# Optimization experiments

Measured on AMD Instinct MI355X. Metric: run time of the kernel, lower is better.

The kernel has to match this reference:

```python
import jax, jax.numpy as jnp
import numpy as np

B, C, L = 128, 1, 4096


def setup_inputs() -> dict:
    key = jax.random.key(0)
    x_0 = jax.random.normal(key, (B, C, L), dtype=jnp.float32)
    return {"x_0": x_0}


def reference(x_0):
    # Original: per-sample F.conv1d(x, flip(x), padding=L-1).
    # Cross-correlation with a flipped kernel == full linear convolution:
    #   out[b, t] = sum_c sum_i x[b,c,i] * x[b,c,t-i],  t in [0, 2L-2]
    # Vectorized over batch and channels via vmap; summed over channels
    # (conv1d contracts input channels against the weight's channel dim).
    conv = jax.vmap(jax.vmap(lambda a: jnp.convolve(a, a, mode='full')))(x_0)  # [B, C, 2L-1]
    return conv.sum(axis=1)[:, None, :]  # [B, 1, 2L-1]
```

## Files before the change

### kernel.cpp

```cpp
#include <hip/hip_runtime.h>

#define LL    4096
#define OUTL  8191
#define FPAD  272
#define NPDW  2336
#define CB1   2352
#define RB    4704
#define BTOP  5887
#define NGUP  992
#define LDSDW 9824
#define UNRL  17

typedef short v8s __attribute__((ext_vector_type(8)));
typedef float v4f __attribute__((ext_vector_type(4)));

__device__ __forceinline__ unsigned bf16b(float f) {
    unsigned u = __builtin_bit_cast(unsigned, f);
    u += 0x7fff + ((u >> 16) & 1);
    return u >> 16;
}
__device__ __forceinline__ unsigned pk(float lo, float hi) {
    return bf16b(lo) | (bf16b(hi) << 16);
}
__device__ __forceinline__ int swz(int g) { return g ^ (((g >> 3) & 3) << 1); }

__global__ __launch_bounds__(512, 4)
void selfconv_mfma7(const float* __restrict__ xg, float* __restrict__ outg) {
    __shared__ unsigned lds[LDSDW];
    const int tid = threadIdx.x;
    const int blk = blockIdx.x;
    const int b   = blk & 127;
    const int id  = blk >> 7;
    const int rg  = (id == 0) ? 0 : (id == 1) ? 3 : (id == 2) ? 1 : 2;
    const int T0  = rg << 11;
    const float* __restrict__ xb = xg + b * LL;

#pragma unroll
    for (int rr = 0; rr < 2; ++rr) {
        int w = tid + rr * 512;
        if (w < 584) {
            int E = 8 * w - FPAD;
            float e0,e1,e2,e3,e4,e5,e6,e7,e8;
            if (E >= 0 && E + 8 < LL) {
                float4 fa = *(const float4*)(xb + E);
                float4 fb = *(const float4*)(xb + E + 4);
                e0=fa.x; e1=fa.y; e2=fa.z; e3=fa.w;
                e4=fb.x; e5=fb.y; e6=fb.z; e7=fb.w; e8=xb[E+8];
            } else {
                float t[9];
#pragma unroll
                for (int k = 0; k < 9; ++k) {
                    int e = E + k;
                    t[k] = (e >= 0 && e < LL) ? xb[e] : 0.f;
                }
                e0=t[0]; e1=t[1]; e2=t[2]; e3=t[3]; e4=t[4];
                e5=t[5]; e6=t[6]; e7=t[7]; e8=t[8];
            }
            unsigned p0 = pk(e0, e1), p1 = pk(e2, e3);
            unsigned p2 = pk(e4, e5), p3 = pk(e6, e7);
            unsigned b8 = bf16b(e8);
            uint4 d0{p0, p1, p2, p3};
            uint4 d1{(p0 >> 16) | (p1 << 16), (p1 >> 16) | (p2 << 16),
                     (p2 >> 16) | (p3 << 16), (p3 >> 16) | (b8 << 16)};
            *(uint4*)&lds[4 * w]       = d0;
            *(uint4*)&lds[CB1 + 4 * w] = d1;
        }
    }
    {
        int g = 224 + tid;
        int x0 = BTOP - 7 - 8 * g;
        float4 fa = *(const float4*)(xb + x0);
        float4 fb = *(const float4*)(xb + x0 + 4);
        uint4 o{pk(fb.w, fb.z), pk(fb.y, fb.x), pk(fa.w, fa.z), pk(fa.y, fa.x)};
        *(uint4*)&lds[RB + 4 * swz(g)] = o;
    }
    if (tid < 480) {
        int u = (tid < 224) ? tid : tid + 512;
        *(uint4*)&lds[RB + 4 * u] = uint4{0, 0, 0, 0};
    }
    __syncthreads();

    const int wv = tid >> 6, lane = tid & 63, ln16 = lane & 15, q = lane >> 4;

    int mn = 0x7fffffff, mx = -0x7fffffff;
#pragma unroll
    for (int u = 0; u < 2; ++u)
#pragma unroll
        for (int v = 0; v < 4; ++v) {
            int base = T0 + 256 * u + 512 * v;
            int iLo = base - (LL - 1); if (iLo < 0) iLo = 0;
            int iHi = base + 255;      if (iHi > LL - 1) iHi = LL - 1;
            int a = iLo - 256 * u; if (a < mn) mn = a;
            int c2 = iHi - 256 * u; if (c2 > mx) mx = c2;
        }
    const int base_   = mn - 15;
    const int i0start = base_ - ((base_ - 1) & 7);
    const int nch     = ((mx - i0start) >> 5) + 1;
    const int nw      = (nch - wv + 7) >> 3;
    const int i0w     = i0start + 32 * wv;

    const int s0p = i0w + ln16 + 8 * q + FPAD;
    const int aw  = (s0p >> 1) + ((s0p & 1) ? CB1 : 0);
    const int g3 = (4352 - T0 + i0w - 16 * ln16 + 8 * q) >> 3;
    const int bw = RB + 4 * swz(g3);

    v4f a00{0,0,0,0}, a01{0,0,0,0}, a02{0,0,0,0}, a03{0,0,0,0};
    v4f a10{0,0,0,0}, a11{0,0,0,0}, a12{0,0,0,0}, a13{0,0,0,0};

    auto mkA = [](const unsigned* p) {
        union { unsigned x[4]; v8s s; } z;
        z.x[0] = p[0]; z.x[1] = p[1]; z.x[2] = p[2]; z.x[3] = p[3];
        return z.s;
    };
    auto mkB = [](uint4 v) {
        union { unsigned x[4]; v8s s; } z;
        z.x[0] = v.x; z.x[1] = v.y; z.x[2] = v.z; z.x[3] = v.w; return z.s;
    };

    uint4 Hb[8];
    unsigned Ab[3][4];
#pragma unroll
    for (int j = 0; j < 7; ++j) Hb[j] = *(const uint4*)&lds[bw + 128 * j];
    Hb[7] = uint4{0, 0, 0, 0};
#pragma unroll
    for (int k = 0; k < 4; ++k) {
        Ab[0][k] = lds[aw + k];
        Ab[1][k] = lds[aw + 128 + k];
        Ab[2][k] = 0u;
    }

#pragma unroll
    for (int t = 0; t < UNRL; ++t) {
        if (t < nw) {
            if (t + 1 < nw) {
                Hb[(t + 7) & 7] = *(const uint4*)&lds[bw + 128 * (t + 7)];
                const int an = aw + 128 * (t + 2);
#pragma unroll
                for (int k = 0; k < 4; ++k) Ab[(t + 2) % 3][k] = lds[an + k];
            }
            v8s A0 = mkA(Ab[t % 3]);
            v8s A1 = mkA(Ab[(t + 1) % 3]);
            v8s B3 = mkB(Hb[t & 7]),       B2 = mkB(Hb[(t + 2) & 7]);
            v8s B1 = mkB(Hb[(t + 4) & 7]), B0 = mkB(Hb[(t + 6) & 7]);
            __builtin_amdgcn_s_setprio(1);
            a03 = __builtin_amdgcn_mfma_f32_16x16x32_bf16(A0, B3, a03, 0, 0, 0);
            a13 = __builtin_amdgcn_mfma_f32_16x16x32_bf16(A1, B3, a13, 0, 0, 0);
            a02 = __builtin_amdgcn_mfma_f32_16x16x32_bf16(A0, B2, a02, 0, 0, 0);
            a12 = __builtin_amdgcn_mfma_f32_16x16x32_bf16(A1, B2, a12, 0, 0, 0);
            a01 = __builtin_amdgcn_mfma_f32_16x16x32_bf16(A0, B1, a01, 0, 0, 0);
            a11 = __builtin_amdgcn_mfma_f32_16x16x32_bf16(A1, B1, a11, 0, 0, 0);
            a00 = __builtin_amdgcn_mfma_f32_16x16x32_bf16(A0, B0, a00, 0, 0, 0);
            a10 = __builtin_amdgcn_mfma_f32_16x16x32_bf16(A1, B0, a10, 0, 0, 0);
            __builtin_amdgcn_s_setprio(0);
        }
    }

    float* fs = (float*)lds;
    __syncthreads();
    if (wv >= 4) {
        int sb = (wv - 4) * 2304 + lane * 36;
        *(v4f*)&fs[sb]      = a00; *(v4f*)&fs[sb + 4]  = a10;
        *(v4f*)&fs[sb + 8]  = a01; *(v4f*)&fs[sb + 12] = a11;
        *(v4f*)&fs[sb + 16] = a02; *(v4f*)&fs[sb + 20] = a12;
        *(v4f*)&fs[sb + 24] = a03; *(v4f*)&fs[sb + 28] = a13;
    }
    __syncthreads();
    if (wv < 4) {
        int sb = wv * 2304 + lane * 36;
        a00 += *(const v4f*)&fs[sb];      a10 += *(const v4f*)&fs[sb + 4];
        a01 += *(const v4f*)&fs[sb + 8];  a11 += *(const v4f*)&fs[sb + 12];
        a02 += *(const v4f*)&fs[sb + 16]; a12 += *(const v4f*)&fs[sb + 20];
        a03 += *(const v4f*)&fs[sb + 24]; a13 += *(const v4f*)&fs[sb + 28];
    }
    __syncthreads();
    if (wv >= 1 && wv < 4) {
        int sb = (wv - 1) * 2304 + lane * 36;
        *(v4f*)&fs[sb]      = a00; *(v4f*)&fs[sb + 4]  = a10;
        *(v4f*)&fs[sb + 8]  = a01; *(v4f*)&fs[sb + 12] = a11;
        *(v4f*)&fs[sb + 16] = a02; *(v4f*)&fs[sb + 20] = a12;
        *(v4f*)&fs[sb + 24] = a03; *(v4f*)&fs[sb + 28] = a13;
    }
    __syncthreads();
    if (wv == 0) {
#pragma unroll
        for (int s = 0; s < 3; ++s) {
            int sb = s * 2304 + lane * 36;
            a00 += *(const v4f*)&fs[sb];      a10 += *(const v4f*)&fs[sb + 4];
            a01 += *(const v4f*)&fs[sb + 8];  a11 += *(const v4f*)&fs[sb + 12];
            a02 += *(const v4f*)&fs[sb + 16]; a12 += *(const v4f*)&fs[sb + 20];
            a03 += *(const v4f*)&fs[sb + 24]; a13 += *(const v4f*)&fs[sb + 28];
        }
        float* __restrict__ ob = outg + b * OUTL;
        const v4f* accs[8] = {&a00, &a10, &a01, &a11, &a02, &a12, &a03, &a13};
#pragma unroll
        for (int uv = 0; uv < 8; ++uv) {
            int u = uv & 1, v = uv >> 1;
            int tilebase = T0 + 256 * u + 512 * v;
            int tb = tilebase + 4 * q + 16 * ln16;
            v4f a = *accs[uv];
            if (tilebase + 255 < OUTL) {
                *(v4f*)&ob[tb] = a;
            } else {
#pragma unroll
                for (int r2 = 0; r2 < 4; ++r2)
                    if (tb + r2 < OUTL) ob[tb + r2] = a[r2];
            }
        }
    }
}

extern "C" void kernel_launch(void* const* d_in, const int* in_sizes, int n_in,
                              void* d_out, int out_size, void* d_ws, size_t ws_size,
                              hipStream_t stream) {
    const float* x = (const float*)d_in[0];
    float* out = (float*)d_out;
    selfconv_mfma7<<<dim3(512), dim3(512), 0, stream>>>(x, out);
}
```

Measured before the change: 61.29 us.

## Replace serial tree reduction with all-wave parallel LDS reduction and store

The cross-wave accumulator reduction goes from a two-stage tree that ended with wave 0 doing all output stores to a single LDS dump by all eight waves. Each wave then sums one output tile across the eight partials and writes it to global memory. This removes two barriers and spreads the reduction and store work over every wave. It also rewrites the operand register buffers as v8s vectors. LDS grows to 64 KB per block, which may limit how many blocks fit per CU.

Measured after the change: 60.86 us. Within noise of the previous version (-0.7%).

```diff
diff --git a/kernel.cpp b/kernel.cpp
--- a/kernel.cpp
+++ b/kernel.cpp
@@ -7,8 +7,7 @@
 #define CB1   2352
 #define RB    4704
 #define BTOP  5887
-#define NGUP  992
-#define LDSDW 9824
+#define LDSDW 16384
 #define UNRL  17
 
 typedef short v8s __attribute__((ext_vector_type(8)));
@@ -25,7 +24,7 @@
 __device__ __forceinline__ int swz(int g) { return g ^ (((g >> 3) & 3) << 1); }
 
 __global__ __launch_bounds__(512, 4)
-void selfconv_mfma7(const float* __restrict__ xg, float* __restrict__ outg) {
+void selfconv_mfma8(const float* __restrict__ xg, float* __restrict__ outg) {
     __shared__ unsigned lds[LDSDW];
     const int tid = threadIdx.x;
     const int blk = blockIdx.x;
@@ -107,41 +106,31 @@
     v4f a00{0,0,0,0}, a01{0,0,0,0}, a02{0,0,0,0}, a03{0,0,0,0};
     v4f a10{0,0,0,0}, a11{0,0,0,0}, a12{0,0,0,0}, a13{0,0,0,0};
 
-    auto mkA = [](const unsigned* p) {
+    auto ldA = [&](int addr) -> v8s {
         union { unsigned x[4]; v8s s; } z;
-        z.x[0] = p[0]; z.x[1] = p[1]; z.x[2] = p[2]; z.x[3] = p[3];
+        z.x[0] = lds[addr];     z.x[1] = lds[addr + 1];
+        z.x[2] = lds[addr + 2]; z.x[3] = lds[addr + 3];
         return z.s;
     };
-    auto mkB = [](uint4 v) {
-        union { unsigned x[4]; v8s s; } z;
-        z.x[0] = v.x; z.x[1] = v.y; z.x[2] = v.z; z.x[3] = v.w; return z.s;
-    };
 
-    uint4 Hb[8];
-    unsigned Ab[3][4];
+    v8s Hs[8];
+    v8s Ah[3];
 #pragma unroll
-    for (int j = 0; j < 7; ++j) Hb[j] = *(const uint4*)&lds[bw + 128 * j];
-    Hb[7] = uint4{0, 0, 0, 0};
-#pragma unroll
-    for (int k = 0; k < 4; ++k) {
-        Ab[0][k] = lds[aw + k];
-        Ab[1][k] = lds[aw + 128 + k];
-        Ab[2][k] = 0u;
-    }
+    for (int j = 0; j < 7; ++j) Hs[j] = *(const v8s*)&lds[bw + 128 * j];
+    Ah[0] = ldA(aw);
+    Ah[1] = ldA(aw + 128);
 
 #pragma unroll
     for (int t = 0; t < UNRL; ++t) {
         if (t < nw) {
             if (t + 1 < nw) {
-                Hb[(t + 7) & 7] = *(const uint4*)&lds[bw + 128 * (t + 7)];
-                const int an = aw + 128 * (t + 2);
-#pragma unroll
-                for (int k = 0; k < 4; ++k) Ab[(t + 2) % 3][k] = lds[an + k];
+                Hs[(t + 7) & 7] = *(const v8s*)&lds[bw + 128 * (t + 7)];
+                Ah[(t + 2) % 3] = ldA(aw + 128 * (t + 2));
             }
-            v8s A0 = mkA(Ab[t % 3]);
-            v8s A1 = mkA(Ab[(t + 1) % 3]);
-            v8s B3 = mkB(Hb[t & 7]),       B2 = mkB(Hb[(t + 2) & 7]);
-            v8s B1 = mkB(Hb[(t + 4) & 7]), B0 = mkB(Hb[(t + 6) & 7]);
+            v8s A0 = Ah[t % 3];
+            v8s A1 = Ah[(t + 1) % 3];
+            v8s B3 = Hs[t & 7],       B2 = Hs[(t + 2) & 7];
+            v8s B1 = Hs[(t + 4) & 7], B0 = Hs[(t + 6) & 7];
             __builtin_amdgcn_s_setprio(1);
             a03 = __builtin_amdgcn_mfma_f32_16x16x32_bf16(A0, B3, a03, 0, 0, 0);
             a13 = __builtin_amdgcn_mfma_f32_16x16x32_bf16(A1, B3, a13, 0, 0, 0);
@@ -157,54 +146,31 @@
 
     float* fs = (float*)lds;
     __syncthreads();
-    if (wv >= 4) {
-        int sb = (wv - 4) * 2304 + lane * 36;
-        *(v4f*)&fs[sb]      = a00; *(v4f*)&fs[sb + 4]  = a10;
-        *(v4f*)&fs[sb + 8]  = a01; *(v4f*)&fs[sb + 12] = a11;
-        *(v4f*)&fs[sb + 16] = a02; *(v4f*)&fs[sb + 20] = a12;
-        *(v4f*)&fs[sb + 24] = a03; *(v4f*)&fs[sb + 28] = a13;
+    {
+        const int lb = wv * 256 + lane * 4;
+        *(v4f*)&fs[0 * 2048 + lb] = a00; *(v4f*)&fs[1 * 2048 + lb] = a10;
+        *(v4f*)&fs[2 * 2048 + lb] = a01; *(v4f*)&fs[3 * 2048 + lb] = a11;
+        *(v4f*)&fs[4 * 2048 + lb] = a02; *(v4f*)&fs[5 * 2048 + lb] = a12;
+        *(v4f*)&fs[6 * 2048 + lb] = a03; *(v4f*)&fs[7 * 2048 + lb] = a13;
     }
     __syncthreads();
-    if (wv < 4) {
-        int sb = wv * 2304 + lane * 36;
-        a00 += *(const v4f*)&fs[sb];      a10 += *(const v4f*)&fs[sb + 4];
-        a01 += *(const v4f*)&fs[sb + 8];  a11 += *(const v4f*)&fs[sb + 12];
-        a02 += *(const v4f*)&fs[sb + 16]; a12 += *(const v4f*)&fs[sb + 20];
-        a03 += *(const v4f*)&fs[sb + 24]; a13 += *(const v4f*)&fs[sb + 28];
-    }
-    __syncthreads();
-    if (wv >= 1 && wv < 4) {
-        int sb = (wv - 1) * 2304 + lane * 36;
-        *(v4f*)&fs[sb]      = a00; *(v4f*)&fs[sb + 4]  = a10;
-        *(v4f*)&fs[sb + 8]  = a01; *(v4f*)&fs[sb + 12] = a11;
-        *(v4f*)&fs[sb + 16] = a02; *(v4f*)&fs[sb + 20] = a12;
-        *(v4f*)&fs[sb + 24] = a03; *(v4f*)&fs[sb + 28] = a13;
-    }
-    __syncthreads();
-    if (wv == 0) {
+    {
+        v4f s{0, 0, 0, 0};
+        const int tb0 = wv * 2048 + lane * 4;
 #pragma unroll
-        for (int s = 0; s < 3; ++s) {
-            int sb = s * 2304 + lane * 36;
-            a00 += *(const v4f*)&fs[sb];      a10 += *(const v4f*)&fs[sb + 4];
-            a01 += *(const v4f*)&fs[sb + 8];  a11 += *(const v4f*)&fs[sb + 12];
-            a02 += *(const v4f*)&fs[sb + 16]; a12 += *(const v4f*)&fs[sb + 20];
-            a03 += *(const v4f*)&fs[sb + 24]; a13 += *(const v4f*)&fs[sb + 28];
-        }
+        for (int w = 0; w < 8; ++w)
+            s += *(const v4f*)&fs[tb0 + w * 256];
+
+        const int u = wv & 1, v = wv >> 1;
+        const int tilebase = T0 + 256 * u + 512 * v;
+        const int tb = tilebase + 16 * ln16 + 4 * q;
         float* __restrict__ ob = outg + b * OUTL;
-        const v4f* accs[8] = {&a00, &a10, &a01, &a11, &a02, &a12, &a03, &a13};
+        if (tilebase + 255 < OUTL) {
+            *(v4f*)&ob[tb] = s;
+        } else {
 #pragma unroll
-        for (int uv = 0; uv < 8; ++uv) {
-            int u = uv & 1, v = uv >> 1;
-            int tilebase = T0 + 256 * u + 512 * v;
-            int tb = tilebase + 4 * q + 16 * ln16;
-            v4f a = *accs[uv];
-            if (tilebase + 255 < OUTL) {
-                *(v4f*)&ob[tb] = a;
-            } else {
-#pragma unroll
-                for (int r2 = 0; r2 < 4; ++r2)
-                    if (tb + r2 < OUTL) ob[tb + r2] = a[r2];
-            }
+            for (int r2 = 0; r2 < 4; ++r2)
+                if (tb + r2 < OUTL) ob[tb + r2] = s[r2];
         }
     }
 }
@@ -214,5 +180,5 @@
                               hipStream_t stream) {
     const float* x = (const float*)d_in[0];
     float* out = (float*)d_out;
-    selfconv_mfma7<<<dim3(512), dim3(512), 0, stream>>>(x, out);
+    selfconv_mfma8<<<dim3(512), dim3(512), 0, stream>>>(x, out);
 }
```
